# Kernel tuning notes

Hardware: AMD Instinct MI355X
Metric: run time of the kernel (lower is better)

## Reference

```python
import jax, jax.numpy as jnp
import numpy as np
from jax.scipy.special import digamma, gammaln

NUM_CLASSES = 3
FOCAL_GAMMA = 2.0
LABEL_SMOOTHING = 0.1
EVIDENTIAL_W = 0.1
CONTRASTIVE_W = 0.1
BOUNDARY_W = 0.15
TRIPLET_W = 0.1
QUALITY_W = 0.1
TRIPLET_MARGIN = 1.5


def setup_inputs() -> dict:
    key = jax.random.key(0)
    k1, k2, k3 = jax.random.split(key, 3)
    B, D = 4096, 512
    logits = jax.random.normal(k1, (B, NUM_CLASSES), dtype=jnp.float32)
    targets = jax.random.randint(k2, (B,), 0, 3)
    features = jax.random.normal(k3, (B, D), dtype=jnp.float32)
    alpha = jax.random.uniform(jax.random.fold_in(key, 7), (B, NUM_CLASSES), dtype=jnp.float32)
    focal_alpha = jnp.array([1.0, 2.0, 1.5], dtype=jnp.float32)
    class_weights = jnp.array([1.0, 2.0, 1.5], dtype=jnp.float32)
    return {"logits": logits, "targets": targets, "features": features,
            "alpha": alpha, "epoch": 1, "focal_alpha": focal_alpha,
            "class_weights": class_weights}


def reference(logits, targets, features, alpha, epoch, focal_alpha, class_weights):
    B = logits.shape[0]
    C = NUM_CLASSES

    # ---- focal loss (label-smoothed CE, torch semantics) ----
    logp = jax.nn.log_softmax(logits, axis=1)                      # [B,C]
    nll = -jnp.take_along_axis(logp, targets[:, None], axis=1)[:, 0]
    ce_ls = (1.0 - LABEL_SMOOTHING) * nll + LABEL_SMOOTHING * (-logp.mean(axis=1))
    pt = jnp.exp(-ce_ls)
    focal = (focal_alpha[targets] * (1.0 - pt) ** FOCAL_GAMMA * ce_ls).mean()

    # ---- weighted CE (torch weighted mean: sum(w*nll)/sum(w)) ----
    w = class_weights[targets]
    ce = (w * nll).sum() / w.sum()

    # ---- enhanced boundary loss ----
    probs = jax.nn.softmax(logits, axis=1)
    real = targets == 0
    semi = targets == 1
    syn = targets == 2
    rb = jnp.where(real, probs[:, 1] + 0.6 * probs[:, 2], 0.0).sum()
    sb = jnp.where(syn, probs[:, 1] + 0.4 * probs[:, 0], 0.0).sum()
    mb = jnp.where(semi, 1.0 - probs[:, 1] + 0.3 * (probs[:, 0] + probs[:, 2]), 0.0).sum()
    boundary = (rb + sb + 4.5 * mb) / (B + 1e-8)

    total = 0.4 * focal + 0.3 * ce + BOUNDARY_W * boundary

    # ---- normalized features and pairwise cosine-sim matrix ----
    norms = jnp.linalg.norm(features, axis=1, keepdims=True)
    f = features / jnp.maximum(norms, 1e-12)
    sim = f @ f.T                                                  # [B,B]
    same = targets[:, None] == targets[None, :]
    eye = jnp.eye(B, dtype=bool)

    # ---- enhanced contrastive loss ----
    pos = jnp.where(same, (1.0 - sim) ** 2, 0.0).sum()
    neg = jnp.where(~same, jnp.clip(sim - 0.2, 0.0) ** 2, 0.0).sum()
    semi_pair = semi[:, None] & semi[None, :]
    semi_l = jnp.where(semi_pair, (1.0 - sim) ** 2, 0.0).sum()
    contrastive = (pos + neg + 4.0 * semi_l) / (B * B + 1e-8)

    # ---- enhanced triplet loss (batch-hard, vectorized) ----
    d2 = jnp.clip(2.0 - 2.0 * sim, 0.0)
    dist = jnp.sqrt(jnp.where(eye, 1.0, d2))  # diag masked; safe sqrt
    pos_mask = same & ~eye
    neg_mask = ~same
    hp = jnp.max(jnp.where(pos_mask, dist, -jnp.inf), axis=1)
    hn = jnp.min(jnp.where(neg_mask, dist, jnp.inf), axis=1)
    valid = pos_mask.any(axis=1) & neg_mask.any(axis=1)
    margin = TRIPLET_MARGIN * jnp.where(targets == 1, 2.5, 1.0)
    tl = jax.nn.relu(hp - hn + margin)
    cnt = valid.sum()
    triplet = jnp.where(cnt > 0,
                        jnp.where(valid, tl, 0.0).sum() / jnp.maximum(cnt, 1),
                        0.0)

    # ---- quality-invariant loss (upper-tri same-class pairs) ----
    upper = jnp.triu(jnp.ones((B, B), dtype=bool), k=1)
    qmask = same & upper
    npairs = qmask.sum()
    q = jnp.where(qmask, (1.0 - sim) ** 2, 0.0).sum() / jnp.maximum(npairs, 1)
    frac2 = syn.astype(jnp.float32).mean()
    q = q * jnp.where(syn.sum() > 0, 1.0 + 2.5 * frac2, 1.0)
    quality = jnp.where(npairs > 0, q, 0.0)

    # ---- evidential loss ----
    onehot = jax.nn.one_hot(targets, C, dtype=jnp.float32)
    S = alpha.sum(axis=1, keepdims=True) + 1e-8
    likelihood = (onehot * (digamma(S) - digamma(alpha + 1e-8))).sum(axis=1)
    at = onehot + (1.0 - onehot) * alpha
    ats = at.sum(axis=1) + 1e-8
    kl = (gammaln(ats) - gammaln(at + 1e-8).sum(axis=1)
          + ((at - 1.0) * (digamma(at + 1e-8) - digamma(ats[:, None] + 1e-8))).sum(axis=1))
    annealing = min(1.0, (epoch / 25.0) ** 2)
    evidential = likelihood.mean() + annealing * 0.2 * kl.mean()

    total = (total + CONTRASTIVE_W * contrastive + TRIPLET_W * triplet
             + QUALITY_W * quality + EVIDENTIAL_W * evidential)
    return total
```

## Files before the change

### kernel.cpp

```cpp
#include <hip/hip_runtime.h>
#include <hip/hip_bf16.h>
#include <cstdint>

typedef __attribute__((ext_vector_type(8))) __bf16 bf8;
typedef __attribute__((ext_vector_type(4))) float f32x4;

#if defined(__has_builtin)
#if __has_builtin(__builtin_amdgcn_global_load_lds)
#define USE_GLL 1
#endif
#endif
#ifndef USE_GLL
#define USE_GLL 0
#endif

#if USE_GLL
__device__ __forceinline__ void gll16(const __bf16* g, __bf16* l){
  __builtin_amdgcn_global_load_lds(
      (const __attribute__((address_space(1))) void*)g,
      (__attribute__((address_space(3))) void*)l, 16, 0, 0);
}
#endif

__device__ __forceinline__ unsigned mapf(float x){
  unsigned u = __float_as_uint(x);
  return (u & 0x80000000u) ? ~u : (u | 0x80000000u);
}
__device__ __forceinline__ float unmapf(unsigned u){
  return __uint_as_float((u & 0x80000000u) ? (u & 0x7FFFFFFFu) : ~u);
}

__device__ float digammaf_(float x){
  float r = 0.f;
  while (x < 6.f){ r -= 1.f/x; x += 1.f; }
  float inv = 1.f/x, inv2 = inv*inv;
  r += logf(x) - 0.5f*inv
     - inv2*(0.08333333333f - inv2*(0.008333333333f - inv2*0.003968253968f));
  return r;
}

__global__ __launch_bounds__(256) void k_prep(const float* __restrict__ feat,
    __bf16* __restrict__ fb,
    const float* __restrict__ logits, const int* __restrict__ targets,
    const float* __restrict__ alpha,  const float* __restrict__ fa,
    const float* __restrict__ cw, int B, int D,
    float* __restrict__ psum, unsigned* __restrict__ pcnt,
    unsigned* rowMinU, unsigned* rowMaxU){
  int bid = blockIdx.x, tid = threadIdx.x;
  int wave = tid >> 6, lane = tid & 63;

  int row = bid*4 + wave;
  if (row < B){
    const float* src = feat + (size_t)row*D;
    float ss = 0.f;
    for (int c = lane*4; c < D; c += 64*4){
      float4 v = *(const float4*)(src + c);
      ss += v.x*v.x + v.y*v.y + v.z*v.z + v.w*v.w;
    }
    #pragma unroll
    for (int off=32; off; off>>=1) ss += __shfl_xor(ss, off);
    float inv = 1.f / fmaxf(sqrtf(ss), 1e-12f);
    __bf16* dst = fb + (size_t)row*D;
    for (int c = lane*8; c < D; c += 64*8){
      float4 v0 = *(const float4*)(src + c);
      float4 v1 = *(const float4*)(src + c + 4);
      bf8 o;
      o[0]=(__bf16)(v0.x*inv); o[1]=(__bf16)(v0.y*inv);
      o[2]=(__bf16)(v0.z*inv); o[3]=(__bf16)(v0.w*inv);
      o[4]=(__bf16)(v1.x*inv); o[5]=(__bf16)(v1.y*inv);
      o[6]=(__bf16)(v1.z*inv); o[7]=(__bf16)(v1.w*inv);
      *(bf8*)(dst + c) = o;
    }
  }

  int SB = B >> 8;
  if (bid >= SB) return;

  int i = bid*256 + tid;
  rowMinU[i] = 0xFFFFFFFFu; rowMaxU[i] = 0u;

  float l0=logits[3*i], l1=logits[3*i+1], l2=logits[3*i+2];
  int t = targets[i];
  float m = fmaxf(l0, fmaxf(l1,l2));
  float e0=expf(l0-m), e1=expf(l1-m), e2=expf(l2-m);
  float se = e0+e1+e2;
  float lse = m + logf(se);
  float lp0=l0-lse, lp1=l1-lse, lp2=l2-lse;
  float lpt = (t==0)?lp0:((t==1)?lp1:lp2);
  float nll = -lpt;
  float ce_ls = 0.9f*nll + 0.1f*(-(lp0+lp1+lp2)*(1.f/3.f));
  float pt = expf(-ce_ls);
  float om = 1.f - pt;
  float focal_i = fa[t]*om*om*ce_ls;
  float w = cw[t];
  float ce_n = w*nll, ce_d = w;
  float p0=e0/se, p1=e1/se, p2=e2/se;
  float bnd;
  if (t==0)      bnd = p1 + 0.6f*p2;
  else if (t==2) bnd = p1 + 0.4f*p0;
  else           bnd = 4.5f*(1.f - p1 + 0.3f*(p0+p2));
  float a0=alpha[3*i], a1=alpha[3*i+1], a2=alpha[3*i+2];
  float S = a0+a1+a2 + 1e-8f;
  float at_ = (t==0)?a0:((t==1)?a1:a2);
  float lik = digammaf_(S) - digammaf_(at_ + 1e-8f);
  float b0 = (t==0)?1.f:a0, b1 = (t==1)?1.f:a1, b2 = (t==2)?1.f:a2;
  float ats = b0+b1+b2 + 1e-8f;
  float psa = digammaf_(ats + 1e-8f);
  float kl = lgammaf(ats)
     - (lgammaf(b0+1e-8f)+lgammaf(b1+1e-8f)+lgammaf(b2+1e-8f))
     + (b0-1.f)*(digammaf_(b0+1e-8f)-psa)
     + (b1-1.f)*(digammaf_(b1+1e-8f)-psa)
     + (b2-1.f)*(digammaf_(b2+1e-8f)-psa);

  unsigned long long m0 = __ballot(t==0);
  unsigned long long m1 = __ballot(t==1);
  unsigned long long m2 = __ballot(t==2);
  #pragma unroll
  for (int off=32; off; off>>=1){
    focal_i += __shfl_xor(focal_i, off);
    ce_n    += __shfl_xor(ce_n, off);
    ce_d    += __shfl_xor(ce_d, off);
    bnd     += __shfl_xor(bnd, off);
    lik     += __shfl_xor(lik, off);
    kl      += __shfl_xor(kl, off);
  }
  if (lane == 0){
    int slot = bid*4 + wave;
    psum[slot*8+0]=focal_i; psum[slot*8+1]=ce_n; psum[slot*8+2]=ce_d;
    psum[slot*8+3]=bnd;     psum[slot*8+4]=lik;  psum[slot*8+5]=kl;
    pcnt[slot*4+0]=(unsigned)__popcll(m0);
    pcnt[slot*4+1]=(unsigned)__popcll(m1);
    pcnt[slot*4+2]=(unsigned)__popcll(m2);
  }
}

__global__ __launch_bounds__(256, 6) void k_pairs(const __bf16* __restrict__ fb,
    const int* __restrict__ targets, int B, int D,
    float* __restrict__ pairPart, unsigned* rowMinU, unsigned* rowMaxU){
  __shared__ __bf16 sA[2][2048];
  __shared__ __bf16 sB[2][2048];
  __shared__ int sRT[64];
  __shared__ int sCT[64];
  __shared__ float sred[4][4];

  int t = blockIdx.x;
  int bx = (int)((sqrtf(8.f*(float)t + 1.f) - 1.f)*0.5f);
  while ((bx+1)*(bx+2)/2 <= t) bx++;
  while (bx*(bx+1)/2 > t) bx--;
  int by = t - bx*(bx+1)/2;
  bool isDiag = (by == bx);
  int rowBase = by*64, colBase = bx*64;

  int tid = threadIdx.x, lane = tid & 63, wave = tid >> 6;
  int wr = wave >> 1, wc = wave & 1;
  int quad = lane >> 4, l16 = lane & 15;

  if (tid < 64)       sRT[tid] = targets[rowBase + tid];
  else if (tid < 128) sCT[tid-64] = targets[colBase + tid - 64];

  int srow = tid >> 2;
  int scb  = (tid & 3) ^ ((srow >> 1) & 3);
  const __bf16* gA = fb + (size_t)(rowBase + srow)*D + scb*8;
  const __bf16* gB = fb + (size_t)(colBase + srow)*D + scb*8;
  int wofs = wave*512;

  int offA[2], offB[2];
  #pragma unroll
  for (int mi=0; mi<2; mi++){
    int R = wr*32 + mi*16 + l16;
    offA[mi] = R*32 + ((quad ^ ((R>>1)&3))*8);
  }
  #pragma unroll
  for (int ni=0; ni<2; ni++){
    int R = wc*32 + ni*16 + l16;
    offB[ni] = R*32 + ((quad ^ ((R>>1)&3))*8);
  }

  f32x4 C[2][2] = {};
  int NIT = D/32;

#if USE_GLL
  #define STAGE(buf, k0) do{ gll16(gA + (k0), &sA[buf][wofs]); \
                             gll16(gB + (k0), &sB[buf][wofs]); }while(0)
#else
  #define STAGE(buf, k0) do{ *(bf8*)&sA[buf][tid*8] = *(const bf8*)(gA + (k0)); \
                             *(bf8*)&sB[buf][tid*8] = *(const bf8*)(gB + (k0)); }while(0)
#endif

  STAGE(0, 0);

  #define COMPUTE(buf) do{ \
    bf8 aF0 = *(const bf8*)(&sA[buf][offA[0]]); \
    bf8 aF1 = *(const bf8*)(&sA[buf][offA[1]]); \
    bf8 bF0 = *(const bf8*)(&sB[buf][offB[0]]); \
    bf8 bF1 = *(const bf8*)(&sB[buf][offB[1]]); \
    C[0][0] = __builtin_amdgcn_mfma_f32_16x16x32_bf16(aF0, bF0, C[0][0], 0,0,0); \
    C[0][1] = __builtin_amdgcn_mfma_f32_16x16x32_bf16(aF0, bF1, C[0][1], 0,0,0); \
    C[1][0] = __builtin_amdgcn_mfma_f32_16x16x32_bf16(aF1, bF0, C[1][0], 0,0,0); \
    C[1][1] = __builtin_amdgcn_mfma_f32_16x16x32_bf16(aF1, bF1, C[1][1], 0,0,0); \
  }while(0)

  for (int it=0; it<NIT; it+=2){
    __syncthreads();
    STAGE(1, (it+1)*32);
    COMPUTE(0);
    __syncthreads();
    if (it+2 < NIT) STAGE(0, (it+2)*32);
    COMPUTE(1);
  }

  int tcol[2];
  #pragma unroll
  for (int ni=0; ni<2; ni++) tcol[ni] = sCT[wc*32 + ni*16 + l16];

  float pos=0.f, neg=0.f, semi=0.f, diag=0.f;
  float cmin[2], cmax[2];
  #pragma unroll
  for (int ni=0; ni<2; ni++){ cmin[ni]=2.f; cmax[ni]=-2.f; }

  #pragma unroll
  for (int mi=0; mi<2; mi++){
    #pragma unroll
    for (int r=0; r<4; r++){
      int rl = wr*32 + mi*16 + quad*4 + r;
      int row = rowBase + rl;
      int tr = sRT[rl];
      float vmin = 2.f, vmax = -2.f;
      #pragma unroll
      for (int ni=0; ni<2; ni++){
        int col = colBase + wc*32 + ni*16 + l16;
        float s = C[mi][ni][r];
        if (tr == tcol[ni]){
          float omv = 1.f - s;
          float q = omv*omv;
          pos += q;
          if (tr == 1) semi += q;
          if (row == col) diag += q;
          else {
            vmin = fminf(vmin, s);
            cmin[ni] = fminf(cmin[ni], s);
          }
        } else {
          float c0 = fmaxf(s - 0.2f, 0.f);
          neg += c0*c0;
          vmax = fmaxf(vmax, s);
          cmax[ni] = fmaxf(cmax[ni], s);
        }
      }
      #pragma unroll
      for (int off=1; off<16; off<<=1){
        vmin = fminf(vmin, __shfl_xor(vmin, off));
        vmax = fmaxf(vmax, __shfl_xor(vmax, off));
      }
      if (l16 == 0){
        atomicMin(&rowMinU[row], mapf(vmin));
        atomicMax(&rowMaxU[row], mapf(vmax));
      }
    }
  }

  if (!isDiag){
    #pragma unroll
    for (int ni=0; ni<2; ni++){
      float cn = cmin[ni], cx = cmax[ni];
      cn = fminf(cn, __shfl_xor(cn, 16)); cn = fminf(cn, __shfl_xor(cn, 32));
      cx = fmaxf(cx, __shfl_xor(cx, 16)); cx = fmaxf(cx, __shfl_xor(cx, 32));
      if (quad == 0){
        int col = colBase + wc*32 + ni*16 + l16;
        atomicMin(&rowMinU[col], mapf(cn));
        atomicMax(&rowMaxU[col], mapf(cx));
      }
    }
  }

  #pragma unroll
  for (int off=32; off; off>>=1){
    pos  += __shfl_xor(pos, off);
    neg  += __shfl_xor(neg, off);
    semi += __shfl_xor(semi, off);
    diag += __shfl_xor(diag, off);
  }
  if (lane == 0){ sred[wave][0]=pos; sred[wave][1]=neg; sred[wave][2]=semi; sred[wave][3]=diag; }
  __syncthreads();
  if (tid == 0){
    float fac = isDiag ? 1.f : 2.f;
    float p=0,n=0,s2=0,d=0;
    for (int w2=0; w2<4; w2++){ p+=sred[w2][0]; n+=sred[w2][1]; s2+=sred[w2][2]; d+=sred[w2][3]; }
    pairPart[blockIdx.x*4+0] = p*fac;
    pairPart[blockIdx.x*4+1] = n*fac;
    pairPart[blockIdx.x*4+2] = s2*fac;
    pairPart[blockIdx.x*4+3] = d;
  }
}

__global__ __launch_bounds__(256) void k_final(const int* __restrict__ targets,
    const int* __restrict__ epoch_p, int B, int SB, int nblk,
    const float* __restrict__ pairPart, const float* __restrict__ psum,
    const unsigned* __restrict__ pcnt,
    const unsigned* rowMinU, const unsigned* rowMaxU, float* out){
  __shared__ float tot[6];
  __shared__ unsigned cn[3];
  __shared__ float ptot[4];
  int tid = threadIdx.x;
  int nslots = SB*4;
  int wave = tid>>6, lane = tid&63;

  if (tid < 64){
    float v0=0,v1=0,v2=0,v3=0,v4=0,v5=0;
    int c0=0,c1=0,c2=0;
    for (int s=tid; s<nslots; s+=64){
      v0+=psum[s*8+0]; v1+=psum[s*8+1]; v2+=psum[s*8+2];
      v3+=psum[s*8+3]; v4+=psum[s*8+4]; v5+=psum[s*8+5];
      c0+=(int)pcnt[s*4+0]; c1+=(int)pcnt[s*4+1]; c2+=(int)pcnt[s*4+2];
    }
    #pragma unroll
    for (int off=32; off; off>>=1){
      v0+=__shfl_xor(v0,off); v1+=__shfl_xor(v1,off); v2+=__shfl_xor(v2,off);
      v3+=__shfl_xor(v3,off); v4+=__shfl_xor(v4,off); v5+=__shfl_xor(v5,off);
      c0+=__shfl_xor(c0,off); c1+=__shfl_xor(c1,off); c2+=__shfl_xor(c2,off);
    }
    if (tid == 0){
      tot[0]=v0; tot[1]=v1; tot[2]=v2; tot[3]=v3; tot[4]=v4; tot[5]=v5;
      cn[0]=(unsigned)c0; cn[1]=(unsigned)c1; cn[2]=(unsigned)c2;
    }
  }

  {
    float p=0,n=0,s2=0,d=0;
    for (int s=tid; s<nblk; s+=256){
      p += pairPart[s*4+0]; n += pairPart[s*4+1];
      s2+= pairPart[s*4+2]; d += pairPart[s*4+3];
    }
    #pragma unroll
    for (int off=32; off; off>>=1){
      p+=__shfl_xor(p,off); n+=__shfl_xor(n,off);
      s2+=__shfl_xor(s2,off); d+=__shfl_xor(d,off);
    }
    __shared__ float pw[4][4];
    if (lane==0){ pw[wave][0]=p; pw[wave][1]=n; pw[wave][2]=s2; pw[wave][3]=d; }
    __syncthreads();
    if (tid==0){
      float a=0,b=0,c=0,e=0;
      for (int w2=0; w2<4; w2++){ a+=pw[w2][0]; b+=pw[w2][1]; c+=pw[w2][2]; e+=pw[w2][3]; }
      ptot[0]=a; ptot[1]=b; ptot[2]=c; ptot[3]=e;
    }
  }
  __syncthreads();
  int n0=(int)cn[0], n1=(int)cn[1], n2=(int)cn[2];

  float tsum = 0.f, tcnt = 0.f;
  for (int i = tid; i < B; i += 256){
    int t = targets[i];
    int nt = (t==0)?n0:((t==1)?n1:n2);
    if (nt - 1 > 0 && B - nt > 0){
      float mn = unmapf(rowMinU[i]);
      float mx = unmapf(rowMaxU[i]);
      float hp = sqrtf(fmaxf(2.f - 2.f*mn, 0.f));
      float hn = sqrtf(fmaxf(2.f - 2.f*mx, 0.f));
      float margin = 1.5f * ((t==1) ? 2.5f : 1.f);
      float tl = fmaxf(hp - hn + margin, 0.f);
      tsum += tl; tcnt += 1.f;
    }
  }
  #pragma unroll
  for (int off=32; off; off>>=1){ tsum += __shfl_xor(tsum, off); tcnt += __shfl_xor(tcnt, off); }
  __shared__ float sb[4][2];
  if (lane==0){ sb[wave][0]=tsum; sb[wave][1]=tcnt; }
  __syncthreads();
  if (tid==0){
    float ts=0, tn=0;
    for (int w2=0;w2<4;w2++){ ts+=sb[w2][0]; tn+=sb[w2][1]; }
    float triplet = (tn > 0.f) ? ts / fmaxf(tn, 1.f) : 0.f;
    float pos=ptot[0], neg=ptot[1], semi=ptot[2], diag=ptot[3];
    float Bf = (float)B;
    float focal = tot[0] / Bf;
    float ce = tot[1] / tot[2];
    float boundary = tot[3] / (Bf + 1e-8f);
    float contrastive = (pos + neg + 4.f*semi) / (Bf*Bf + 1e-8f);
    long long npl = ((long long)n0*(n0-1) + (long long)n1*(n1-1) + (long long)n2*(n2-1))/2;
    float qsum = (pos - diag) * 0.5f;
    float q = qsum / (float)(npl > 0 ? npl : 1);
    if (n2 > 0) q *= (1.f + 2.5f * ((float)n2 / Bf));
    float quality = (npl > 0) ? q : 0.f;
    int ep = epoch_p[0];
    float er = (float)ep / 25.f;
    float ann = fminf(1.f, er*er);
    float evidential = tot[4]/Bf + ann*0.2f*tot[5]/Bf;
    float total = 0.4f*focal + 0.3f*ce + 0.15f*boundary
                + 0.1f*contrastive + 0.1f*triplet + 0.1f*quality + 0.1f*evidential;
    out[0] = total;
  }
}

extern "C" void kernel_launch(void* const* d_in, const int* in_sizes, int n_in,
                              void* d_out, int out_size, void* d_ws, size_t ws_size,
                              hipStream_t stream){
  const float* logits   = (const float*)d_in[0];
  const int*   targets  = (const int*)d_in[1];
  const float* features = (const float*)d_in[2];
  const float* alpha    = (const float*)d_in[3];
  const int*   epoch    = (const int*)d_in[4];
  const float* fa       = (const float*)d_in[5];
  const float* cw       = (const float*)d_in[6];
  int B = in_sizes[1];
  int D = in_sizes[2] / B;
  int SB = B >> 8;
  int T  = B / 64;
  int nblk = T*(T+1)/2;

  char* ws = (char*)d_ws;
  unsigned* pcnt     = (unsigned*)(ws);
  float*    psum     = (float*)(ws + 16384);
  float*    pairPart = (float*)(ws + 32768);
  unsigned* rowMinU  = (unsigned*)(ws + 131072);
  unsigned* rowMaxU  = (unsigned*)(ws + 131072 + (size_t)B*4);
  __bf16*   fb       = (__bf16*)(ws + 131072 + (size_t)B*8);

  k_prep <<<B/4, 256, 0, stream>>>(features, fb, logits, targets, alpha, fa, cw,
                                   B, D, psum, pcnt, rowMinU, rowMaxU);
  k_pairs<<<nblk, 256, 0, stream>>>(fb, targets, B, D, pairPart, rowMinU, rowMaxU);
  k_final<<<1, 256, 0, stream>>>(targets, epoch, B, SB, nblk, pairPart, psum, pcnt,
                                 rowMinU, rowMaxU, (float*)d_out);
}
```

Baseline: 129.4 us.

## Compute each 64x64 pair tile with a single wave and drop block barriers

The pairwise similarity kernel now runs one 64-thread wave per 64x64 tile instead of four waves each owning a 32x32 sub-tile. Each wave holds a 4x4 grid of MFMA accumulators, so every LDS fragment it loads feeds more matrix ops. Because only one wave touches the shared buffers, the __syncthreads barriers and the shared-memory staging of targets and partial sums are removed. The trade-off is four times fewer waves for latency hiding, higher register pressure, and reliance on the compiler's wait counts to order the async global-to-LDS copies before they are read.

```diff
diff --git a/kernel.cpp b/kernel.cpp
--- a/kernel.cpp
+++ b/kernel.cpp
@@ -134,14 +134,11 @@
   }
 }
 
-__global__ __launch_bounds__(256, 6) void k_pairs(const __bf16* __restrict__ fb,
+__global__ __launch_bounds__(64, 3) void k_pairs(const __bf16* __restrict__ fb,
     const int* __restrict__ targets, int B, int D,
     float* __restrict__ pairPart, unsigned* rowMinU, unsigned* rowMaxU){
   __shared__ __bf16 sA[2][2048];
   __shared__ __bf16 sB[2][2048];
-  __shared__ int sRT[64];
-  __shared__ int sCT[64];
-  __shared__ float sred[4][4];
 
   int t = blockIdx.x;
   int bx = (int)((sqrtf(8.f*(float)t + 1.f) - 1.f)*0.5f);
@@ -151,84 +148,91 @@
   bool isDiag = (by == bx);
   int rowBase = by*64, colBase = bx*64;
 
-  int tid = threadIdx.x, lane = tid & 63, wave = tid >> 6;
-  int wr = wave >> 1, wc = wave & 1;
+  int lane = threadIdx.x;
   int quad = lane >> 4, l16 = lane & 15;
 
-  if (tid < 64)       sRT[tid] = targets[rowBase + tid];
-  else if (tid < 128) sCT[tid-64] = targets[colBase + tid - 64];
-
-  int srow = tid >> 2;
-  int scb  = (tid & 3) ^ ((srow >> 1) & 3);
-  const __bf16* gA = fb + (size_t)(rowBase + srow)*D + scb*8;
-  const __bf16* gB = fb + (size_t)(colBase + srow)*D + scb*8;
-  int wofs = wave*512;
-
-  int offA[2], offB[2];
-  #pragma unroll
-  for (int mi=0; mi<2; mi++){
-    int R = wr*32 + mi*16 + l16;
+  const __bf16* gA[4]; const __bf16* gB[4];
+  #pragma unroll
+  for (int j=0; j<4; j++){
+    int row = j*16 + (lane >> 2);
+    int gcb = (lane & 3) ^ ((row >> 1) & 3);
+    gA[j] = fb + (size_t)(rowBase + row)*D + gcb*8;
+    gB[j] = fb + (size_t)(colBase + row)*D + gcb*8;
+  }
+
+  int offA[4], offB[4];
+  #pragma unroll
+  for (int mi=0; mi<4; mi++){
+    int R = mi*16 + l16;
     offA[mi] = R*32 + ((quad ^ ((R>>1)&3))*8);
-  }
-  #pragma unroll
-  for (int ni=0; ni<2; ni++){
-    int R = wc*32 + ni*16 + l16;
-    offB[ni] = R*32 + ((quad ^ ((R>>1)&3))*8);
-  }
-
-  f32x4 C[2][2] = {};
+    offB[mi] = offA[mi];
+  }
+
+  f32x4 C[4][4] = {};
+
+#if USE_GLL
+  #define STAGE(buf, k0) do{ \
+    gll16(gA[0] + (k0), &sA[buf][0*512]); \
+    gll16(gA[1] + (k0), &sA[buf][1*512]); \
+    gll16(gA[2] + (k0), &sA[buf][2*512]); \
+    gll16(gA[3] + (k0), &sA[buf][3*512]); \
+    gll16(gB[0] + (k0), &sB[buf][0*512]); \
+    gll16(gB[1] + (k0), &sB[buf][1*512]); \
+    gll16(gB[2] + (k0), &sB[buf][2*512]); \
+    gll16(gB[3] + (k0), &sB[buf][3*512]); \
+  }while(0)
+#else
+  #define STAGE(buf, k0) do{ \
+    _Pragma("unroll") \
+    for (int j=0; j<4; j++){ \
+      *(bf8*)&sA[buf][j*512 + lane*8] = *(const bf8*)(gA[j] + (k0)); \
+      *(bf8*)&sB[buf][j*512 + lane*8] = *(const bf8*)(gB[j] + (k0)); \
+    } \
+  }while(0)
+#endif
+
+  #define COMPUTE(buf) do{ \
+    bf8 aF[4], bF[4]; \
+    _Pragma("unroll") \
+    for (int mi=0; mi<4; mi++) aF[mi] = *(const bf8*)(&sA[buf][offA[mi]]); \
+    _Pragma("unroll") \
+    for (int ni=0; ni<4; ni++) bF[ni] = *(const bf8*)(&sB[buf][offB[ni]]); \
+    _Pragma("unroll") \
+    for (int mi=0; mi<4; mi++) \
+      _Pragma("unroll") \
+      for (int ni=0; ni<4; ni++) \
+        C[mi][ni] = __builtin_amdgcn_mfma_f32_16x16x32_bf16(aF[mi], bF[ni], C[mi][ni], 0,0,0); \
+  }while(0)
+
   int NIT = D/32;
-
-#if USE_GLL
-  #define STAGE(buf, k0) do{ gll16(gA + (k0), &sA[buf][wofs]); \
-                             gll16(gB + (k0), &sB[buf][wofs]); }while(0)
-#else
-  #define STAGE(buf, k0) do{ *(bf8*)&sA[buf][tid*8] = *(const bf8*)(gA + (k0)); \
-                             *(bf8*)&sB[buf][tid*8] = *(const bf8*)(gB + (k0)); }while(0)
-#endif
-
   STAGE(0, 0);
-
-  #define COMPUTE(buf) do{ \
-    bf8 aF0 = *(const bf8*)(&sA[buf][offA[0]]); \
-    bf8 aF1 = *(const bf8*)(&sA[buf][offA[1]]); \
-    bf8 bF0 = *(const bf8*)(&sB[buf][offB[0]]); \
-    bf8 bF1 = *(const bf8*)(&sB[buf][offB[1]]); \
-    C[0][0] = __builtin_amdgcn_mfma_f32_16x16x32_bf16(aF0, bF0, C[0][0], 0,0,0); \
-    C[0][1] = __builtin_amdgcn_mfma_f32_16x16x32_bf16(aF0, bF1, C[0][1], 0,0,0); \
-    C[1][0] = __builtin_amdgcn_mfma_f32_16x16x32_bf16(aF1, bF0, C[1][0], 0,0,0); \
-    C[1][1] = __builtin_amdgcn_mfma_f32_16x16x32_bf16(aF1, bF1, C[1][1], 0,0,0); \
-  }while(0)
-
   for (int it=0; it<NIT; it+=2){
-    __syncthreads();
     STAGE(1, (it+1)*32);
     COMPUTE(0);
-    __syncthreads();
     if (it+2 < NIT) STAGE(0, (it+2)*32);
     COMPUTE(1);
   }
 
-  int tcol[2];
-  #pragma unroll
-  for (int ni=0; ni<2; ni++) tcol[ni] = sCT[wc*32 + ni*16 + l16];
+  int tcol[4];
+  #pragma unroll
+  for (int ni=0; ni<4; ni++) tcol[ni] = targets[colBase + ni*16 + l16];
 
   float pos=0.f, neg=0.f, semi=0.f, diag=0.f;
-  float cmin[2], cmax[2];
-  #pragma unroll
-  for (int ni=0; ni<2; ni++){ cmin[ni]=2.f; cmax[ni]=-2.f; }
-
-  #pragma unroll
-  for (int mi=0; mi<2; mi++){
+  float cmin[4], cmax[4];
+  #pragma unroll
+  for (int ni=0; ni<4; ni++){ cmin[ni]=2.f; cmax[ni]=-2.f; }
+
+  #pragma unroll
+  for (int mi=0; mi<4; mi++){
     #pragma unroll
     for (int r=0; r<4; r++){
-      int rl = wr*32 + mi*16 + quad*4 + r;
+      int rl = mi*16 + quad*4 + r;
       int row = rowBase + rl;
-      int tr = sRT[rl];
+      int tr = targets[row];
       float vmin = 2.f, vmax = -2.f;
       #pragma unroll
-      for (int ni=0; ni<2; ni++){
-        int col = colBase + wc*32 + ni*16 + l16;
+      for (int ni=0; ni<4; ni++){
+        int col = colBase + ni*16 + l16;
         float s = C[mi][ni][r];
         if (tr == tcol[ni]){
           float omv = 1.f - s;
@@ -261,12 +265,12 @@
 
   if (!isDiag){
     #pragma unroll
-    for (int ni=0; ni<2; ni++){
+    for (int ni=0; ni<4; ni++){
       float cn = cmin[ni], cx = cmax[ni];
       cn = fminf(cn, __shfl_xor(cn, 16)); cn = fminf(cn, __shfl_xor(cn, 32));
       cx = fmaxf(cx, __shfl_xor(cx, 16)); cx = fmaxf(cx, __shfl_xor(cx, 32));
       if (quad == 0){
-        int col = colBase + wc*32 + ni*16 + l16;
+        int col = colBase + ni*16 + l16;
         atomicMin(&rowMinU[col], mapf(cn));
         atomicMax(&rowMaxU[col], mapf(cx));
       }
@@ -280,16 +284,12 @@
     semi += __shfl_xor(semi, off);
     diag += __shfl_xor(diag, off);
   }
-  if (lane == 0){ sred[wave][0]=pos; sred[wave][1]=neg; sred[wave][2]=semi; sred[wave][3]=diag; }
-  __syncthreads();
-  if (tid == 0){
+  if (lane == 0){
     float fac = isDiag ? 1.f : 2.f;
-    float p=0,n=0,s2=0,d=0;
-    for (int w2=0; w2<4; w2++){ p+=sred[w2][0]; n+=sred[w2][1]; s2+=sred[w2][2]; d+=sred[w2][3]; }
-    pairPart[blockIdx.x*4+0] = p*fac;
-    pairPart[blockIdx.x*4+1] = n*fac;
-    pairPart[blockIdx.x*4+2] = s2*fac;
-    pairPart[blockIdx.x*4+3] = d;
+    pairPart[blockIdx.x*4+0] = pos*fac;
+    pairPart[blockIdx.x*4+1] = neg*fac;
+    pairPart[blockIdx.x*4+2] = semi*fac;
+    pairPart[blockIdx.x*4+3] = diag;
   }
 }
 
@@ -418,7 +418,7 @@
 
   k_prep <<<B/4, 256, 0, stream>>>(features, fb, logits, targets, alpha, fa, cw,
                                    B, D, psum, pcnt, rowMinU, rowMaxU);
-  k_pairs<<<nblk, 256, 0, stream>>>(fb, targets, B, D, pairPart, rowMinU, rowMaxU);
+  k_pairs<<<nblk, 64, 0, stream>>>(fb, targets, B, D, pairPart, rowMinU, rowMaxU);
   k_final<<<1, 256, 0, stream>>>(targets, epoch, B, SB, nblk, pairPart, psum, pcnt,
                                  rowMinU, rowMaxU, (float*)d_out);
 }
```

New measurement: 127.8 us. About the same (-1.2%).
